# Optimization experiments

Hardware: AMD Instinct MI355X
Metric: run time of the kernel (lower is better)

Reference implementation:

```python
import jax, jax.numpy as jnp
import numpy as np

D = 128
LN_EPS = 1e-5

def _mlp2(x, W1, b1, W2, b2):
    return jax.nn.silu(x @ W1 + b1) @ W2 + b2

def setup_inputs() -> dict:
    key = jax.random.key(0)
    ks = jax.random.split(key, 20)
    B, N = 2, 512
    inp = {
        'scalar_features': jax.random.normal(ks[0], (B, N, D), jnp.float32),
        'vector_features': jax.random.normal(ks[1], (B, N, 3), jnp.float32),
        'positions': jax.random.normal(ks[2], (B, N, 3), jnp.float32),
        'pair_mask': jnp.ones((B, N, N), jnp.float32),
        'conservation': jax.random.uniform(ks[3], (B, N, 1), jnp.float32),
    }
    s = 0.02
    inp['eW1'] = jax.random.normal(ks[4], (2 * D + 4, D), jnp.float32) * s
    inp['eb1'] = jnp.zeros((D,), jnp.float32)
    inp['eW2'] = jax.random.normal(ks[5], (D, D), jnp.float32) * s
    inp['eb2'] = jnp.zeros((D,), jnp.float32)
    inp['sW1'] = jax.random.normal(ks[6], (2 * D, D), jnp.float32) * s
    inp['sb1'] = jnp.zeros((D,), jnp.float32)
    inp['sW2'] = jax.random.normal(ks[7], (D, D), jnp.float32) * s
    inp['sb2'] = jnp.zeros((D,), jnp.float32)
    inp['vW1'] = jax.random.normal(ks[8], (D, D), jnp.float32) * s
    inp['vb1'] = jnp.zeros((D,), jnp.float32)
    inp['vW2'] = jax.random.normal(ks[9], (D, 1), jnp.float32) * s
    inp['vb2'] = jnp.zeros((1,), jnp.float32)
    inp['ln_w'] = jnp.ones((D,), jnp.float32)
    inp['ln_b'] = jnp.zeros((D,), jnp.float32)
    return inp

def reference(scalar_features, vector_features, positions, pair_mask, conservation,
              eW1, eb1, eW2, eb2, sW1, sb1, sW2, sb2, vW1, vb1, vW2, vb2, ln_w, ln_b):
    N = scalar_features.shape[-2]
    # rel[b,i,j] = pos[b,i] - pos[b,j]
    rel = positions[..., :, None, :] - positions[..., None, :, :]          # [B,N,N,3]
    dist = jnp.maximum(jnp.linalg.norm(rel, axis=-1, keepdims=True), 1e-8)  # [B,N,N,1]
    direction = rel / dist
    feat_i = jnp.broadcast_to(scalar_features[..., :, None, :], scalar_features.shape[:-2] + (N, N, D))
    feat_j = jnp.broadcast_to(scalar_features[..., None, :, :], scalar_features.shape[:-2] + (N, N, D))
    cons_i = jnp.broadcast_to(conservation[..., :, None, :], conservation.shape[:-2] + (N, N, 1))
    cons_j = jnp.broadcast_to(conservation[..., None, :, :], conservation.shape[:-2] + (N, N, 1))
    edge_input = jnp.concatenate([feat_i, feat_j, dist, cons_i, cons_j, pair_mask[..., None]], axis=-1)
    edge_hidden = _mlp2(edge_input, eW1, eb1, eW2, eb2)                    # [B,N,N,D]
    edge_weights = jax.nn.sigmoid(edge_hidden.mean(axis=-1)) * pair_mask   # [B,N,N]
    message_scalar = (edge_hidden * edge_weights[..., None]).sum(axis=-2)  # sum over j -> [B,N,D]
    upd = _mlp2(jnp.concatenate([scalar_features, message_scalar], axis=-1), sW1, sb1, sW2, sb2)
    x = scalar_features + upd
    mu = x.mean(axis=-1, keepdims=True)
    var = x.var(axis=-1, keepdims=True)
    scalar_out = (x - mu) * jax.lax.rsqrt(var + LN_EPS) * ln_w + ln_b
    vector_gate = _mlp2(edge_hidden, vW1, vb1, vW2, vb2)[..., 0] * edge_weights  # [B,N,N]
    vector_message = (vector_gate[..., None] * direction).sum(axis=-2)           # [B,N,3]
    vector_out = vector_features + vector_message
    return scalar_out, vector_out, edge_weights
```

## Files before the change

### kernel.cpp

```cpp
#include <hip/hip_runtime.h>

#define DD 128
#define NN 512
#define NODES 1024

typedef short bf16x8 __attribute__((ext_vector_type(8)));
typedef float f32x4 __attribute__((ext_vector_type(4)));
typedef float f32x2 __attribute__((ext_vector_type(2)));

__device__ __forceinline__ float sigmoidf_(float x) {
  return __builtin_amdgcn_rcpf(1.f + __expf(-x));
}
__device__ __forceinline__ float siluf_(float x) { return x * sigmoidf_(x); }

__device__ __forceinline__ unsigned short f2bf_(float v) {
  unsigned int u = __float_as_uint(v);
  u += 0x7fffu + ((u >> 16) & 1u);
  return (unsigned short)(u >> 16);
}
__device__ __forceinline__ unsigned cvtpk_(float lo, float hi) {
  unsigned r;
  asm("v_cvt_pk_bf16_f32 %0, %1, %2" : "=v"(r) : "v"(lo), "v"(hi));
  return r;
}
__device__ __forceinline__ float bflo_(unsigned u) { return __uint_as_float(u << 16); }
__device__ __forceinline__ float bfhi_(unsigned u) { return __uint_as_float(u & 0xffff0000u); }

__device__ __forceinline__ f32x2 pk_fma(f32x2 a, f32x2 b, f32x2 c) {
  return __builtin_elementwise_fma(a, b, c);
}
__device__ __forceinline__ f32x2 mk2(float a, float b) { return (f32x2){a, b}; }
__device__ __forceinline__ f32x2 bc2(float a) { return (f32x2){a, a}; }

__device__ __forceinline__ f32x2 silu2_(f32x2 p) {
  f32x2 np = -p;
  f32x2 e;
  e.x = __expf(np.x);
  e.y = __expf(np.y);
  f32x2 den = e + bc2(1.f);
  f32x2 r;
  r.x = __builtin_amdgcn_rcpf(den.x);
  r.y = __builtin_amdgcn_rcpf(den.y);
  return p * r;
}

__global__ __launch_bounds__(128) void prep_kernel(
    const float* __restrict__ sf, const float* __restrict__ cons,
    const float* __restrict__ eW1, const float* __restrict__ eb1,
    const float* __restrict__ eW2, const float* __restrict__ eb2,
    const float* __restrict__ vW1, const float* __restrict__ vb1,
    float* __restrict__ Ag, float* __restrict__ Bvg,
    unsigned short* __restrict__ E2V1T, float* __restrict__ m2,
    float* __restrict__ c1, float* __restrict__ mb)
{
  const int bid = blockIdx.x;
  const int d = threadIdx.x;
  if (bid < NODES) {
    float c = cons[bid];
    float aacc = c * eW1[258*DD + d];
    float bacc = eb1[d] + c * eW1[257*DD + d];
    const float* sfrow = sf + bid*DD;
    #pragma unroll 4
    for (int k = 0; k < DD; ++k) {
      float s = sfrow[k];
      aacc = fmaf(s, eW1[(128+k)*DD + d], aacc);
      bacc = fmaf(s, eW1[k*DD + d], bacc);
    }
    Ag[bid*DD + d]  = aacc;
    Bvg[bid*DD + d] = bacc;
  } else if (bid < NODES + 128) {
    const int k = bid - NODES;
    float acc = 0.f;
    #pragma unroll 4
    for (int t = 0; t < DD; ++t) acc = fmaf(eW2[k*DD + t], vW1[t*DD + d], acc);
    E2V1T[d*DD + (k ^ ((d & 7) << 3))] = f2bf_(acc);
    if (d == 0) {
      float s = 0.f;
      for (int t = 0; t < DD; ++t) s += eW2[k*DD + t];
      m2[k] = s * (1.0f/128.0f);
    }
  } else {
    float acc = vb1[d];
    #pragma unroll 4
    for (int k = 0; k < DD; ++k) acc = fmaf(eb2[k], vW1[k*DD + d], acc);
    c1[d] = acc;
    if (d == 0) {
      float s = 0.f;
      for (int k = 0; k < DD; ++k) s += eb2[k];
      mb[0] = s * (1.0f/128.0f);
    }
  }
}

__global__ __launch_bounds__(256, 2) void edge_kernel(
    const float* __restrict__ sf, const float* __restrict__ vf,
    const float* __restrict__ pos, const float* __restrict__ pm,
    const float* __restrict__ eW1,
    const float* __restrict__ eW2, const float* __restrict__ eb2,
    const float* __restrict__ sW1, const float* __restrict__ sb1,
    const float* __restrict__ sW2, const float* __restrict__ sb2,
    const float* __restrict__ vW2g, const float* __restrict__ vb2g,
    const float* __restrict__ lnw, const float* __restrict__ lnb,
    const float* __restrict__ Ag, const float* __restrict__ Bvg,
    const unsigned short* __restrict__ E2V1Tg, const float* __restrict__ m2g,
    const float* __restrict__ c1g, const float* __restrict__ mbg,
    float* __restrict__ sout, float* __restrict__ vout, float* __restrict__ ewout)
{
  __shared__ __align__(16) unsigned short eTs[128*128];
  __shared__ __align__(16) float BvL[DD], w256L[DD], w259L[DD], m2L[DD];
  __shared__ __align__(16) float c1L[DD], vw2L[DD];
  __shared__ __align__(16) float scr2[1152];
  __shared__ float redS[4], redVx[4], redVy[4], redVz[4], redA[2], redB[2];

  const int tid = threadIdx.x;
  const int ni  = blockIdx.x;
  const int nb  = ni & ~(NN - 1);

  const int l   = tid & 63, w = tid >> 6;
  const int l15 = l & 15,  lg = l >> 4;
  const int d   = tid & 127, sub = tid >> 7;
  const int d0base = lg*8;

  {
    const uint4* src = (const uint4*)E2V1Tg;
    uint4* dst = (uint4*)eTs;
    #pragma unroll
    for (int it = 0; it < 8; ++it) dst[tid + it*256] = src[tid + it*256];
  }
  if (tid < 128) {
    BvL[tid]   = Bvg[(size_t)ni*DD + tid];
    w256L[tid] = eW1[256*DD + tid];
    w259L[tid] = eW1[259*DD + tid];
    m2L[tid]   = m2g[tid];
    c1L[tid]   = c1g[tid];
    vw2L[tid]  = vW2g[tid];
  }
  const float pix = pos[ni*3+0], piy = pos[ni*3+1], piz = pos[ni*3+2];
  const float mbv = mbg[0], vb2v = vb2g[0];

  f32x2 Sp[4][4];
  #pragma unroll
  for (int kk = 0; kk < 4; ++kk)
    #pragma unroll
    for (int m = 0; m < 4; ++m) Sp[kk][m] = (f32x2){0.f, 0.f};
  float vmx = 0.f, vmy = 0.f, vmz = 0.f, swacc = 0.f;

  __syncthreads();

  for (int t = 0; t < 4; ++t) {
    const int row0 = t*128 + w*16 + l15;
    const int row1 = row0 + 64;
    float p0x = pos[(nb + row0)*3 + 0], p0y = pos[(nb + row0)*3 + 1], p0z = pos[(nb + row0)*3 + 2];
    float p1x = pos[(nb + row1)*3 + 0], p1y = pos[(nb + row1)*3 + 1], p1z = pos[(nb + row1)*3 + 2];
    float r0x = pix - p0x, r0y = piy - p0y, r0z = piz - p0z;
    float r1x = pix - p1x, r1y = piy - p1y, r1z = piz - p1z;
    float dist0 = fmaxf(sqrtf(r0x*r0x + r0y*r0y + r0z*r0z), 1e-8f);
    float dist1 = fmaxf(sqrtf(r1x*r1x + r1y*r1y + r1z*r1z), 1e-8f);
    float inv0 = __builtin_amdgcn_rcpf(dist0);
    float inv1 = __builtin_amdgcn_rcpf(dist1);
    float dir0x = r0x*inv0, dir0y = r0y*inv0, dir0z = r0z*inv0;
    float dir1x = r1x*inv1, dir1y = r1y*inv1, dir1z = r1z*inv1;
    float mj0 = pm[(size_t)ni*NN + row0];
    float mj1 = pm[(size_t)ni*NN + row1];

    const f32x2 distp0 = bc2(dist0), distp1 = bc2(dist1);
    const f32x2 mjp0 = bc2(mj0), mjp1 = bc2(mj1);

    uint4 pkA0, pkA1, pkA2, pkA3, pkB0, pkB1, pkB2, pkB3;
    f32x2 dotp0 = {0.f,0.f}, dotp1 = {0.f,0.f};
    const float* ag0 = Ag + (size_t)(nb + row0)*DD;
    const float* ag1 = Ag + (size_t)(nb + row1)*DD;

#define H_PAIR(BP, WAP, WBP, AP, DISTP, MJP) \
    silu2_(pk_fma(MJP, WBP, pk_fma(DISTP, WAP, (BP) + (AP))))

#define A_STEP2(KK, PKA, PKB) {                                                   \
    const int d0 = (KK)*32 + d0base;                                              \
    float4 b0 = *(const float4*)&BvL[d0],   b1 = *(const float4*)&BvL[d0+4];      \
    float4 wa0= *(const float4*)&w256L[d0], wa1= *(const float4*)&w256L[d0+4];    \
    float4 wb0= *(const float4*)&w259L[d0], wb1= *(const float4*)&w259L[d0+4];    \
    float4 m20= *(const float4*)&m2L[d0],   m21= *(const float4*)&m2L[d0+4];      \
    float4 aa0 = *(const float4*)(ag0 + d0), aa1 = *(const float4*)(ag0 + d0 + 4);\
    float4 ba0 = *(const float4*)(ag1 + d0), ba1 = *(const float4*)(ag1 + d0 + 4);\
    f32x2 hA0 = H_PAIR(mk2(b0.x,b0.y), mk2(wa0.x,wa0.y), mk2(wb0.x,wb0.y), mk2(aa0.x,aa0.y), distp0, mjp0); \
    f32x2 hA1 = H_PAIR(mk2(b0.z,b0.w), mk2(wa0.z,wa0.w), mk2(wb0.z,wb0.w), mk2(aa0.z,aa0.w), distp0, mjp0); \
    f32x2 hA2 = H_PAIR(mk2(b1.x,b1.y), mk2(wa1.x,wa1.y), mk2(wb1.x,wb1.y), mk2(aa1.x,aa1.y), distp0, mjp0); \
    f32x2 hA3 = H_PAIR(mk2(b1.z,b1.w), mk2(wa1.z,wa1.w), mk2(wb1.z,wb1.w), mk2(aa1.z,aa1.w), distp0, mjp0); \
    f32x2 hB0 = H_PAIR(mk2(b0.x,b0.y), mk2(wa0.x,wa0.y), mk2(wb0.x,wb0.y), mk2(ba0.x,ba0.y), distp1, mjp1); \
    f32x2 hB1 = H_PAIR(mk2(b0.z,b0.w), mk2(wa0.z,wa0.w), mk2(wb0.z,wb0.w), mk2(ba0.z,ba0.w), distp1, mjp1); \
    f32x2 hB2 = H_PAIR(mk2(b1.x,b1.y), mk2(wa1.x,wa1.y), mk2(wb1.x,wb1.y), mk2(ba1.x,ba1.y), distp1, mjp1); \
    f32x2 hB3 = H_PAIR(mk2(b1.z,b1.w), mk2(wa1.z,wa1.w), mk2(wb1.z,wb1.w), mk2(ba1.z,ba1.w), distp1, mjp1); \
    PKA.x = cvtpk_(hA0.x, hA0.y); PKA.y = cvtpk_(hA1.x, hA1.y);                   \
    PKA.z = cvtpk_(hA2.x, hA2.y); PKA.w = cvtpk_(hA3.x, hA3.y);                   \
    PKB.x = cvtpk_(hB0.x, hB0.y); PKB.y = cvtpk_(hB1.x, hB1.y);                   \
    PKB.z = cvtpk_(hB2.x, hB2.y); PKB.w = cvtpk_(hB3.x, hB3.y);                   \
    dotp0 = pk_fma(hA0, mk2(m20.x,m20.y), dotp0);                                 \
    dotp0 = pk_fma(hA1, mk2(m20.z,m20.w), dotp0);                                 \
    dotp0 = pk_fma(hA2, mk2(m21.x,m21.y), dotp0);                                 \
    dotp0 = pk_fma(hA3, mk2(m21.z,m21.w), dotp0);                                 \
    dotp1 = pk_fma(hB0, mk2(m20.x,m20.y), dotp1);                                 \
    dotp1 = pk_fma(hB1, mk2(m20.z,m20.w), dotp1);                                 \
    dotp1 = pk_fma(hB2, mk2(m21.x,m21.y), dotp1);                                 \
    dotp1 = pk_fma(hB3, mk2(m21.z,m21.w), dotp1); }

    A_STEP2(0, pkA0, pkB0)
    A_STEP2(1, pkA1, pkB1)
    A_STEP2(2, pkA2, pkB2)
    A_STEP2(3, pkA3, pkB3)
#undef A_STEP2
#undef H_PAIR

    float dot0 = dotp0.x + dotp0.y;
    float dot1 = dotp1.x + dotp1.y;
    dot0 += __shfl_xor(dot0, 16);
    dot0 += __shfl_xor(dot0, 32);
    dot1 += __shfl_xor(dot1, 16);
    dot1 += __shfl_xor(dot1, 32);
    const float w0 = mj0 * sigmoidf_(dot0 + mbv);
    const float w1 = mj1 * sigmoidf_(dot1 + mbv);
    if (lg == 0) {
      ewout[(size_t)ni*NN + row0] = w0;
      ewout[(size_t)ni*NN + row1] = w1;
      swacc += w0 + w1;
    }
    const f32x2 w0p = bc2(w0), w1p = bc2(w1);

#define S_STEP2(KK, PKA, PKB) {                                                     \
    Sp[KK][0] = pk_fma(w1p, mk2(bflo_(PKB.x), bfhi_(PKB.x)),                        \
                pk_fma(w0p, mk2(bflo_(PKA.x), bfhi_(PKA.x)), Sp[KK][0]));           \
    Sp[KK][1] = pk_fma(w1p, mk2(bflo_(PKB.y), bfhi_(PKB.y)),                        \
                pk_fma(w0p, mk2(bflo_(PKA.y), bfhi_(PKA.y)), Sp[KK][1]));           \
    Sp[KK][2] = pk_fma(w1p, mk2(bflo_(PKB.z), bfhi_(PKB.z)),                        \
                pk_fma(w0p, mk2(bflo_(PKA.z), bfhi_(PKA.z)), Sp[KK][2]));           \
    Sp[KK][3] = pk_fma(w1p, mk2(bflo_(PKB.w), bfhi_(PKB.w)),                        \
                pk_fma(w0p, mk2(bflo_(PKA.w), bfhi_(PKA.w)), Sp[KK][3])); }

    S_STEP2(0, pkA0, pkB0)
    S_STEP2(1, pkA1, pkB1)
    S_STEP2(2, pkA2, pkB2)
    S_STEP2(3, pkA3, pkB3)
#undef S_STEP2

    const bf16x8 afA0 = __builtin_bit_cast(bf16x8, pkA0);
    const bf16x8 afA1 = __builtin_bit_cast(bf16x8, pkA1);
    const bf16x8 afA2 = __builtin_bit_cast(bf16x8, pkA2);
    const bf16x8 afA3 = __builtin_bit_cast(bf16x8, pkA3);
    const bf16x8 afB0 = __builtin_bit_cast(bf16x8, pkB0);
    const bf16x8 afB1 = __builtin_bit_cast(bf16x8, pkB1);
    const bf16x8 afB2 = __builtin_bit_cast(bf16x8, pkB2);
    const bf16x8 afB3 = __builtin_bit_cast(bf16x8, pkB3);

    f32x2 gp0a = {0.f,0.f}, gp0b = {0.f,0.f};
    f32x2 gp1a = {0.f,0.f}, gp1b = {0.f,0.f};
    #pragma unroll
    for (int ct = 0; ct < 8; ++ct) {
      const int col = ct*16 + l15;
      const int swz = (col & 7) << 3;
      const unsigned short* ecol = &eTs[col*DD];
      bf16x8 bf0 = *(const bf16x8*)&ecol[(  0 + d0base) ^ swz];
      bf16x8 bf1 = *(const bf16x8*)&ecol[( 32 + d0base) ^ swz];
      bf16x8 bf2 = *(const bf16x8*)&ecol[( 64 + d0base) ^ swz];
      bf16x8 bf3 = *(const bf16x8*)&ecol[( 96 + d0base) ^ swz];
      f32x4 c0 = {0.f,0.f,0.f,0.f};
      f32x4 c1v = {0.f,0.f,0.f,0.f};
      c0  = __builtin_amdgcn_mfma_f32_16x16x32_bf16(afA0, bf0, c0, 0, 0, 0);
      c1v = __builtin_amdgcn_mfma_f32_16x16x32_bf16(afB0, bf0, c1v, 0, 0, 0);
      c0  = __builtin_amdgcn_mfma_f32_16x16x32_bf16(afA1, bf1, c0, 0, 0, 0);
      c1v = __builtin_amdgcn_mfma_f32_16x16x32_bf16(afB1, bf1, c1v, 0, 0, 0);
      c0  = __builtin_amdgcn_mfma_f32_16x16x32_bf16(afA2, bf2, c0, 0, 0, 0);
      c1v = __builtin_amdgcn_mfma_f32_16x16x32_bf16(afB2, bf2, c1v, 0, 0, 0);
      c0  = __builtin_amdgcn_mfma_f32_16x16x32_bf16(afA3, bf3, c0, 0, 0, 0);
      c1v = __builtin_amdgcn_mfma_f32_16x16x32_bf16(afB3, bf3, c1v, 0, 0, 0);
      const f32x2 c1p = bc2(c1L[col]);
      const f32x2 vwp = bc2(vw2L[col]);
      gp0a = pk_fma(silu2_(mk2(c0[0],  c0[1])  + c1p), vwp, gp0a);
      gp0b = pk_fma(silu2_(mk2(c0[2],  c0[3])  + c1p), vwp, gp0b);
      gp1a = pk_fma(silu2_(mk2(c1v[0], c1v[1]) + c1p), vwp, gp1a);
      gp1b = pk_fma(silu2_(mk2(c1v[2], c1v[3]) + c1p), vwp, gp1b);
    }
    {
      float g4_0[4] = { gp0a.x, gp0a.y, gp0b.x, gp0b.y };
      float g4_1[4] = { gp1a.x, gp1a.y, gp1b.x, gp1b.y };
      #pragma unroll
      for (int r = 0; r < 4; ++r) {
        float v0 = g4_0[r], v1 = g4_1[r];
        v0 += __shfl_xor(v0, 1);  v1 += __shfl_xor(v1, 1);
        v0 += __shfl_xor(v0, 2);  v1 += __shfl_xor(v1, 2);
        v0 += __shfl_xor(v0, 4);  v1 += __shfl_xor(v1, 4);
        v0 += __shfl_xor(v0, 8);  v1 += __shfl_xor(v1, 8);
        const int srow = lg*4 + r;
        float wr0 = __shfl(w0, srow);
        float wr1 = __shfl(w1, srow);
        float g0 = (v0 + vb2v) * wr0;
        float g1 = (v1 + vb2v) * wr1;
        float d0x = __shfl(dir0x, srow), d0y = __shfl(dir0y, srow), d0z = __shfl(dir0z, srow);
        float d1x = __shfl(dir1x, srow), d1y = __shfl(dir1y, srow), d1z = __shfl(dir1z, srow);
        if (l15 == 0) {
          vmx = fmaf(g0, d0x, fmaf(g1, d1x, vmx));
          vmy = fmaf(g0, d0y, fmaf(g1, d1y, vmy));
          vmz = fmaf(g0, d0z, fmaf(g1, d1z, vmz));
        }
      }
    }
  }

  float* Spart = scr2;
  float* SL    = scr2 + 512;
  float* partA = scr2 + 640;
  float* msgL  = scr2 + 768;
  float* u1L   = scr2 + 896;
  float* xoL   = scr2 + 1024;

  #pragma unroll
  for (int kk = 0; kk < 4; ++kk)
    #pragma unroll
    for (int m = 0; m < 4; ++m) {
      float va = Sp[kk][m].x, vb = Sp[kk][m].y;
      va += __shfl_xor(va, 1);  vb += __shfl_xor(vb, 1);
      va += __shfl_xor(va, 2);  vb += __shfl_xor(vb, 2);
      va += __shfl_xor(va, 4);  vb += __shfl_xor(vb, 4);
      va += __shfl_xor(va, 8);  vb += __shfl_xor(vb, 8);
      Sp[kk][m].x = va; Sp[kk][m].y = vb;
    }
  if (l15 == 0) {
    #pragma unroll
    for (int kk = 0; kk < 4; ++kk)
      #pragma unroll
      for (int m = 0; m < 4; ++m) {
        Spart[w*128 + kk*32 + lg*8 + m*2 + 0] = Sp[kk][m].x;
        Spart[w*128 + kk*32 + lg*8 + m*2 + 1] = Sp[kk][m].y;
      }
  }
  {
    float sw = swacc;
    #pragma unroll
    for (int off = 1; off < 64; off <<= 1) sw += __shfl_xor(sw, off);
    if (l == 0) redS[w] = sw;
  }
  {
    float vx = vmx, vy = vmy, vz = vmz;
    #pragma unroll
    for (int off = 1; off < 64; off <<= 1) {
      vx += __shfl_xor(vx, off);
      vy += __shfl_xor(vy, off);
      vz += __shfl_xor(vz, off);
    }
    if (l == 0) { redVx[w] = vx; redVy[w] = vy; redVz[w] = vz; }
  }
  __syncthreads();
  if (tid < 128) SL[tid] = Spart[tid] + Spart[128+tid] + Spart[256+tid] + Spart[384+tid];
  if (tid == 0) {
    vout[ni*3 + 0] = vf[ni*3 + 0] + redVx[0]+redVx[1]+redVx[2]+redVx[3];
    vout[ni*3 + 1] = vf[ni*3 + 1] + redVy[0]+redVy[1]+redVy[2]+redVy[3];
    vout[ni*3 + 2] = vf[ni*3 + 2] + redVz[0]+redVz[1]+redVz[2]+redVz[3];
  }
  __syncthreads();
  const float sumwv = redS[0] + redS[1] + redS[2] + redS[3];

  float p = 0.f;
  { int k0 = sub*64;
    float pa = 0.f, pb = 0.f;
    #pragma unroll 4
    for (int k = k0; k < k0 + 32; ++k) {
      pa = fmaf(SL[k], eW2[k*DD + d], pa);
      pb = fmaf(SL[k+32], eW2[(k+32)*DD + d], pb);
    }
    p = pa + pb; }
  if (sub) partA[d] = p;
  __syncthreads();
  if (!sub) msgL[d] = p + partA[d] + sumwv * eb2[d];
  __syncthreads();

  float q = 0.f;
  if (!sub) {
    const float* xr = sf + (size_t)ni*DD;
    float qa = 0.f, qb = 0.f;
    #pragma unroll 4
    for (int tt = 0; tt < 64; ++tt) {
      qa = fmaf(xr[tt], sW1[tt*DD + d], qa);
      qb = fmaf(xr[tt+64], sW1[(tt+64)*DD + d], qb);
    }
    q = qa + qb;
  } else {
    float qa = 0.f, qb = 0.f;
    #pragma unroll 4
    for (int tt = 0; tt < 64; ++tt) {
      qa = fmaf(msgL[tt], sW1[(128 + tt)*DD + d], qa);
      qb = fmaf(msgL[tt+64], sW1[(192 + tt)*DD + d], qb);
    }
    q = qa + qb;
  }
  if (sub) partA[d] = q;
  __syncthreads();
  if (!sub) u1L[d] = siluf_(q + partA[d] + sb1[d]);
  __syncthreads();

  float r2 = 0.f;
  { int t0 = sub*64;
    float ra = 0.f, rb = 0.f;
    #pragma unroll 4
    for (int tt = t0; tt < t0 + 32; ++tt) {
      ra = fmaf(u1L[tt], sW2[tt*DD + d], ra);
      rb = fmaf(u1L[tt+32], sW2[(tt+32)*DD + d], rb);
    }
    r2 = ra + rb; }
  if (sub) partA[d] = r2;
  __syncthreads();
  if (!sub) xoL[d] = sf[(size_t)ni*DD + d] + r2 + partA[d] + sb2[d];
  __syncthreads();

  if (tid < 128) {
    float v = xoL[tid];
    float s1 = v, s2 = v*v;
    #pragma unroll
    for (int off = 1; off < 64; off <<= 1) { s1 += __shfl_xor(s1, off); s2 += __shfl_xor(s2, off); }
    if ((tid & 63) == 0) { redA[tid >> 6] = s1; redB[tid >> 6] = s2; }
  }
  __syncthreads();
  if (tid < 128) {
    float s1 = redA[0] + redA[1], s2 = redB[0] + redB[1];
    float mu = s1 * 0.0078125f;
    float var = s2 * 0.0078125f - mu*mu;
    sout[(size_t)ni*DD + tid] = (xoL[tid] - mu) * rsqrtf(var + 1e-5f) * lnw[tid] + lnb[tid];
  }
}

extern "C" void kernel_launch(void* const* d_in, const int* in_sizes, int n_in,
                              void* d_out, int out_size, void* d_ws, size_t ws_size,
                              hipStream_t stream) {
  const float* sf   = (const float*)d_in[0];
  const float* vf   = (const float*)d_in[1];
  const float* pos  = (const float*)d_in[2];
  const float* pm   = (const float*)d_in[3];
  const float* cons = (const float*)d_in[4];
  const float* eW1  = (const float*)d_in[5];
  const float* eb1  = (const float*)d_in[6];
  const float* eW2  = (const float*)d_in[7];
  const float* eb2  = (const float*)d_in[8];
  const float* sW1  = (const float*)d_in[9];
  const float* sb1  = (const float*)d_in[10];
  const float* sW2  = (const float*)d_in[11];
  const float* sb2  = (const float*)d_in[12];
  const float* vW1  = (const float*)d_in[13];
  const float* vb1  = (const float*)d_in[14];
  const float* vW2  = (const float*)d_in[15];
  const float* vb2  = (const float*)d_in[16];
  const float* lnw  = (const float*)d_in[17];
  const float* lnb  = (const float*)d_in[18];

  float* ws   = (float*)d_ws;
  float* Ag   = ws;
  float* Bvg  = ws + 131072;
  float* m2   = ws + 262144;
  float* c1   = ws + 262272;
  float* mb   = ws + 262400;
  unsigned short* E2V1T = (unsigned short*)(ws + 262404);

  float* sout  = (float*)d_out;
  float* vout  = sout + 131072;
  float* ewout = sout + 134144;

  hipLaunchKernelGGL(prep_kernel, dim3(NODES + 129), dim3(128), 0, stream,
                     sf, cons, eW1, eb1, eW2, eb2, vW1, vb1,
                     Ag, Bvg, E2V1T, m2, c1, mb);
  hipLaunchKernelGGL(edge_kernel, dim3(NODES), dim3(256), 0, stream,
                     sf, vf, pos, pm, eW1, eW2, eb2, sW1, sb1, sW2, sb2,
                     vW2, vb2, lnw, lnb, Ag, Bvg, E2V1T, m2, c1, mb,
                     sout, vout, ewout);
}
```

Baseline: 90.59 us.

## Process two nodes per block sharing the staged weight matrix in LDS

Each edge_kernel block now runs 512 threads and handles two nodes, one per 256-thread half. Both halves share a single copy of the bf16 E2V1T weight tile in LDS, which halves the global-to-LDS staging traffic per node. The scratch buffers for the epilogue now reuse the eTs region after an added barrier, which cuts LDS use. In exchange, all barriers now synchronise both halves, and the 512-thread launch bound may tighten register limits.

```diff
diff --git a/kernel.cpp b/kernel.cpp
--- a/kernel.cpp
+++ b/kernel.cpp
@@ -92,7 +92,7 @@
   }
 }
 
-__global__ __launch_bounds__(256, 2) void edge_kernel(
+__global__ __launch_bounds__(512, 2) void edge_kernel(
     const float* __restrict__ sf, const float* __restrict__ vf,
     const float* __restrict__ pos, const float* __restrict__ pm,
     const float* __restrict__ eW1,
@@ -107,34 +107,37 @@
     float* __restrict__ sout, float* __restrict__ vout, float* __restrict__ ewout)
 {
   __shared__ __align__(16) unsigned short eTs[128*128];
-  __shared__ __align__(16) float BvL[DD], w256L[DD], w259L[DD], m2L[DD];
-  __shared__ __align__(16) float c1L[DD], vw2L[DD];
-  __shared__ __align__(16) float scr2[1152];
-  __shared__ float redS[4], redVx[4], redVy[4], redVz[4], redA[2], redB[2];
-
-  const int tid = threadIdx.x;
-  const int ni  = blockIdx.x;
-  const int nb  = ni & ~(NN - 1);
-
-  const int l   = tid & 63, w = tid >> 6;
+  __shared__ __align__(16) float BvL2[2][DD];
+  __shared__ __align__(16) float w256L[DD], w259L[DD], m2L[DD], c1L[DD], vw2L[DD];
+  __shared__ float redS[2][4], redVx[2][4], redVy[2][4], redVz[2][4], redA[2][2], redB[2][2];
+
+  const int tid  = threadIdx.x;
+  const int half = tid >> 8;
+  const int tloc = tid & 255;
+  const int ni   = blockIdx.x*2 + half;
+  const int nb   = ni & ~(NN - 1);
+
+  const int l   = tid & 63, w = tloc >> 6;
   const int l15 = l & 15,  lg = l >> 4;
-  const int d   = tid & 127, sub = tid >> 7;
+  const int d   = tloc & 127, sub = tloc >> 7;
   const int d0base = lg*8;
 
   {
     const uint4* src = (const uint4*)E2V1Tg;
     uint4* dst = (uint4*)eTs;
     #pragma unroll
-    for (int it = 0; it < 8; ++it) dst[tid + it*256] = src[tid + it*256];
+    for (int it = 0; it < 4; ++it) dst[tid + it*512] = src[tid + it*512];
   }
   if (tid < 128) {
-    BvL[tid]   = Bvg[(size_t)ni*DD + tid];
     w256L[tid] = eW1[256*DD + tid];
     w259L[tid] = eW1[259*DD + tid];
     m2L[tid]   = m2g[tid];
     c1L[tid]   = c1g[tid];
     vw2L[tid]  = vW2g[tid];
   }
+  if (tloc < 128) BvL2[half][tloc] = Bvg[(size_t)ni*DD + tloc];
+  const float* BvL = &BvL2[half][0];
+
   const float pix = pos[ni*3+0], piy = pos[ni*3+1], piz = pos[ni*3+2];
   const float mbv = mbg[0], vb2v = vb2g[0];
 
@@ -304,12 +307,14 @@
     }
   }
 
-  float* Spart = scr2;
-  float* SL    = scr2 + 512;
-  float* partA = scr2 + 640;
-  float* msgL  = scr2 + 768;
-  float* u1L   = scr2 + 896;
-  float* xoL   = scr2 + 1024;
+  __syncthreads();
+  float* base  = (float*)eTs + half*2048;
+  float* Spart = base;
+  float* SL    = base + 512;
+  float* partA = base + 640;
+  float* msgL  = base + 768;
+  float* u1L   = base + 896;
+  float* xoL   = base + 1024;
 
   #pragma unroll
   for (int kk = 0; kk < 4; ++kk)
@@ -335,7 +340,7 @@
     float sw = swacc;
     #pragma unroll
     for (int off = 1; off < 64; off <<= 1) sw += __shfl_xor(sw, off);
-    if (l == 0) redS[w] = sw;
+    if (l == 0) redS[half][w] = sw;
   }
   {
     float vx = vmx, vy = vmy, vz = vmz;
@@ -345,17 +350,17 @@
       vy += __shfl_xor(vy, off);
       vz += __shfl_xor(vz, off);
     }
-    if (l == 0) { redVx[w] = vx; redVy[w] = vy; redVz[w] = vz; }
-  }
-  __syncthreads();
-  if (tid < 128) SL[tid] = Spart[tid] + Spart[128+tid] + Spart[256+tid] + Spart[384+tid];
-  if (tid == 0) {
-    vout[ni*3 + 0] = vf[ni*3 + 0] + redVx[0]+redVx[1]+redVx[2]+redVx[3];
-    vout[ni*3 + 1] = vf[ni*3 + 1] + redVy[0]+redVy[1]+redVy[2]+redVy[3];
-    vout[ni*3 + 2] = vf[ni*3 + 2] + redVz[0]+redVz[1]+redVz[2]+redVz[3];
-  }
-  __syncthreads();
-  const float sumwv = redS[0] + redS[1] + redS[2] + redS[3];
+    if (l == 0) { redVx[half][w] = vx; redVy[half][w] = vy; redVz[half][w] = vz; }
+  }
+  __syncthreads();
+  if (tloc < 128) SL[tloc] = Spart[tloc] + Spart[128+tloc] + Spart[256+tloc] + Spart[384+tloc];
+  if (tloc == 0) {
+    vout[ni*3 + 0] = vf[ni*3 + 0] + redVx[half][0]+redVx[half][1]+redVx[half][2]+redVx[half][3];
+    vout[ni*3 + 1] = vf[ni*3 + 1] + redVy[half][0]+redVy[half][1]+redVy[half][2]+redVy[half][3];
+    vout[ni*3 + 2] = vf[ni*3 + 2] + redVz[half][0]+redVz[half][1]+redVz[half][2]+redVz[half][3];
+  }
+  __syncthreads();
+  const float sumwv = redS[half][0] + redS[half][1] + redS[half][2] + redS[half][3];
 
   float p = 0.f;
   { int k0 = sub*64;
@@ -409,19 +414,19 @@
   if (!sub) xoL[d] = sf[(size_t)ni*DD + d] + r2 + partA[d] + sb2[d];
   __syncthreads();
 
-  if (tid < 128) {
-    float v = xoL[tid];
+  if (tloc < 128) {
+    float v = xoL[tloc];
     float s1 = v, s2 = v*v;
     #pragma unroll
     for (int off = 1; off < 64; off <<= 1) { s1 += __shfl_xor(s1, off); s2 += __shfl_xor(s2, off); }
-    if ((tid & 63) == 0) { redA[tid >> 6] = s1; redB[tid >> 6] = s2; }
-  }
-  __syncthreads();
-  if (tid < 128) {
-    float s1 = redA[0] + redA[1], s2 = redB[0] + redB[1];
+    if ((tloc & 63) == 0) { redA[half][tloc >> 6] = s1; redB[half][tloc >> 6] = s2; }
+  }
+  __syncthreads();
+  if (tloc < 128) {
+    float s1 = redA[half][0] + redA[half][1], s2 = redB[half][0] + redB[half][1];
     float mu = s1 * 0.0078125f;
     float var = s2 * 0.0078125f - mu*mu;
-    sout[(size_t)ni*DD + tid] = (xoL[tid] - mu) * rsqrtf(var + 1e-5f) * lnw[tid] + lnb[tid];
+    sout[(size_t)ni*DD + tloc] = (xoL[tloc] - mu) * rsqrtf(var + 1e-5f) * lnw[tloc] + lnb[tloc];
   }
 }
 
@@ -463,7 +468,7 @@
   hipLaunchKernelGGL(prep_kernel, dim3(NODES + 129), dim3(128), 0, stream,
                      sf, cons, eW1, eb1, eW2, eb2, vW1, vb1,
                      Ag, Bvg, E2V1T, m2, c1, mb);
-  hipLaunchKernelGGL(edge_kernel, dim3(NODES), dim3(256), 0, stream,
+  hipLaunchKernelGGL(edge_kernel, dim3(NODES/2), dim3(512), 0, stream,
                      sf, vf, pos, pm, eW1, eW2, eb2, sW1, sb1, sW2, sb2,
                      vW2, vb2, lnw, lnb, Ag, Bvg, E2V1T, m2, c1, mb,
                      sout, vout, ewout);
```

Result: slower. 94.05 us (+3.8%).
